# Optimization experiments

Measured on AMD Instinct MI355X. Metric: run time of the kernel, lower is better.

The kernel has to match this reference:

```python
import jax, jax.numpy as jnp
import numpy as np

B, M, K = 32, 64, 36
DS, DX, DQ, H = 512, 128, 512, 256


def setup_inputs() -> dict:
    key = jax.random.key(0)
    ks = jax.random.split(key, 11)
    sc = lambda fan_in: 1.0 / np.sqrt(fan_in)
    return {
        "s2": jax.random.normal(ks[0], (B, M, DS), jnp.float32),
        "x0": jax.random.normal(ks[1], (B, K, DX), jnp.float32),
        "q": jax.random.normal(ks[2], (B, DQ), jnp.float32),
        # score MLP: Linear(DS+DX+DQ -> H), ReLU, Linear(H -> 1)
        "score_w1": jax.random.normal(ks[3], (DS + DX + DQ, H), jnp.float32) * sc(DS + DX + DQ),
        "score_b1": jax.random.normal(ks[4], (H,), jnp.float32) * 0.01,
        "score_w2": jax.random.normal(ks[5], (H, 1), jnp.float32) * sc(H),
        "score_b2": jax.random.normal(ks[6], (1,), jnp.float32) * 0.01,
        # h MLP: Linear(DS -> H), ReLU, Linear(H -> DX)
        "h_w1": jax.random.normal(ks[7], (DS, H), jnp.float32) * sc(DS),
        "h_b1": jax.random.normal(ks[8], (H,), jnp.float32) * 0.01,
        "h_w2": jax.random.normal(ks[9], (H, DX), jnp.float32) * sc(H),
        "h_b2": jax.random.normal(ks[10], (DX,), jnp.float32) * 0.01,
    }


def reference(s2, x0, q, score_w1, score_b1, score_w2, score_b2, h_w1, h_b1, h_w2, h_b2):
    ds = s2.shape[-1]
    dx = x0.shape[-1]
    # First score Linear over concat [s_exp, x_exp, q_exp] decomposes into
    # block matmuls (same math as Linear on the concat, no 4D concat tensor).
    w_s = score_w1[:ds]            # (DS, H)
    w_x = score_w1[ds:ds + dx]     # (DX, H)
    w_q = score_w1[ds + dx:]       # (DQ, H)
    pre_s = jnp.einsum('bmd,dh->bmh', s2, w_s)   # (b, m, H)
    pre_x = jnp.einsum('bkd,dh->bkh', x0, w_x)   # (b, k, H)
    pre_q = q @ w_q                              # (b, H)
    hidden = jax.nn.relu(pre_s[:, :, None, :] + pre_x[:, None, :, :]
                         + pre_q[:, None, None, :] + score_b1)  # (b, m, k, H)
    logits = jnp.einsum('bmkh,h->bmk', hidden, score_w2[:, 0]) + score_b2[0]
    att = jax.nn.softmax(logits, axis=1)         # softmax over m
    h_s = jax.nn.relu(s2 @ h_w1 + h_b1) @ h_w2 + h_b2  # (b, m, DX)
    agg = jnp.einsum('bmk,bmf->bkf', att, h_s)   # (b, k, DX)
    return jnp.concatenate([x0, agg], axis=-1)   # (b, k, 2*DX)
```

## Files before the change

kernel.cpp:

```cpp
#include <hip/hip_runtime.h>

#define B_  32
#define M_  64
#define K_  36
#define DS_ 512
#define DX_ 128
#define DQ_ 512
#define H_  256

#define ROWS 8

__global__ __launch_bounds__(256) void kern1(
    const float* __restrict__ s2,
    const float* __restrict__ x0,
    const float* __restrict__ q,
    const float* __restrict__ score_w1,
    const float* __restrict__ score_b1,
    const float* __restrict__ h_w1,
    const float* __restrict__ h_b1,
    const float* __restrict__ h_w2,
    float* __restrict__ pre_s,
    float* __restrict__ px,
    float* __restrict__ qpre,
    float* __restrict__ hs)
{
    __shared__ float Ar[ROWS][H_];
    const int t   = threadIdx.x;
    const int bid = blockIdx.x;

    if (bid < 512) {
        const int tile = bid >> 1, mat = bid & 1;
        const float* W  = mat ? h_w1 : score_w1;
        const float* A  = s2 + (size_t)tile * ROWS * DS_;
        const float* Wp = W + t;

        float acc[ROWS];
        #pragma unroll
        for (int r = 0; r < ROWS; ++r) acc[r] = 0.f;

        #pragma unroll 2
        for (int k = 0; k < DS_; k += 4) {
            const float b0 = Wp[(size_t)(k + 0) * H_];
            const float b1 = Wp[(size_t)(k + 1) * H_];
            const float b2 = Wp[(size_t)(k + 2) * H_];
            const float b3 = Wp[(size_t)(k + 3) * H_];
            #pragma unroll
            for (int r = 0; r < ROWS; ++r) {
                const float4 a = *(const float4*)(A + (size_t)r * DS_ + k);
                acc[r] = fmaf(a.x, b0, acc[r]);
                acc[r] = fmaf(a.y, b1, acc[r]);
                acc[r] = fmaf(a.z, b2, acc[r]);
                acc[r] = fmaf(a.w, b3, acc[r]);
            }
        }

        if (!mat) {
            float* dst = pre_s + (size_t)tile * ROWS * H_ + t;
            #pragma unroll
            for (int r = 0; r < ROWS; ++r)
                dst[(size_t)r * H_] = acc[r];
        } else {
            const float b1v = h_b1[t];
            #pragma unroll
            for (int r = 0; r < ROWS; ++r)
                Ar[r][t] = fmaxf(acc[r] + b1v, 0.f);
            __syncthreads();

            const int f  = t & 127;
            const int rh = t >> 7;
            const float* w2p = h_w2 + f;
            float o0 = 0.f, o1 = 0.f, o2 = 0.f, o3 = 0.f;
            #pragma unroll 2
            for (int k = 0; k < H_; k += 4) {
                const float w0 = w2p[(size_t)(k + 0) * DX_];
                const float w1 = w2p[(size_t)(k + 1) * DX_];
                const float w2v = w2p[(size_t)(k + 2) * DX_];
                const float w3 = w2p[(size_t)(k + 3) * DX_];
                const float4 a0 = *(const float4*)&Ar[rh * 4 + 0][k];
                const float4 a1 = *(const float4*)&Ar[rh * 4 + 1][k];
                const float4 a2 = *(const float4*)&Ar[rh * 4 + 2][k];
                const float4 a3 = *(const float4*)&Ar[rh * 4 + 3][k];
                o0 = fmaf(a0.x, w0, o0); o0 = fmaf(a0.y, w1, o0);
                o0 = fmaf(a0.z, w2v, o0); o0 = fmaf(a0.w, w3, o0);
                o1 = fmaf(a1.x, w0, o1); o1 = fmaf(a1.y, w1, o1);
                o1 = fmaf(a1.z, w2v, o1); o1 = fmaf(a1.w, w3, o1);
                o2 = fmaf(a2.x, w0, o2); o2 = fmaf(a2.y, w1, o2);
                o2 = fmaf(a2.z, w2v, o2); o2 = fmaf(a2.w, w3, o2);
                o3 = fmaf(a3.x, w0, o3); o3 = fmaf(a3.y, w1, o3);
                o3 = fmaf(a3.z, w2v, o3); o3 = fmaf(a3.w, w3, o3);
            }
            float* dst = hs + ((size_t)tile * ROWS + rh * 4) * DX_ + f;
            dst[0 * DX_] = o0;
            dst[1 * DX_] = o1;
            dst[2 * DX_] = o2;
            dst[3 * DX_] = o3;
        }

    } else if (bid < 656) {
        const int tile = bid - 512;
        const float* A  = x0 + (size_t)tile * ROWS * DX_;
        const float* Wp = score_w1 + (size_t)DS_ * H_ + t;

        float acc[ROWS];
        #pragma unroll
        for (int r = 0; r < ROWS; ++r) acc[r] = 0.f;

        #pragma unroll 2
        for (int k = 0; k < DX_; k += 4) {
            const float b0 = Wp[(size_t)(k + 0) * H_];
            const float b1 = Wp[(size_t)(k + 1) * H_];
            const float b2 = Wp[(size_t)(k + 2) * H_];
            const float b3 = Wp[(size_t)(k + 3) * H_];
            #pragma unroll
            for (int r = 0; r < ROWS; ++r) {
                const float4 a = *(const float4*)(A + (size_t)r * DX_ + k);
                acc[r] = fmaf(a.x, b0, acc[r]);
                acc[r] = fmaf(a.y, b1, acc[r]);
                acc[r] = fmaf(a.z, b2, acc[r]);
                acc[r] = fmaf(a.w, b3, acc[r]);
            }
        }
        const float b1v = score_b1[t];
        float* dst = px + (size_t)tile * ROWS * H_ + t;
        #pragma unroll
        for (int r = 0; r < ROWS; ++r)
            dst[(size_t)r * H_] = acc[r] + b1v;

    } else {
        const int b = bid - 656;
        const float* qp = q + (size_t)b * DQ_;
        const float* wq = score_w1 + (size_t)(DS_ + DX_) * H_ + t;
        float a0 = 0.f, a1 = 0.f, a2 = 0.f, a3 = 0.f;
        #pragma unroll 2
        for (int d = 0; d < DQ_; d += 4) {
            const float4 q4 = *(const float4*)(qp + d);
            a0 = fmaf(q4.x, wq[(size_t)(d + 0) * H_], a0);
            a1 = fmaf(q4.y, wq[(size_t)(d + 1) * H_], a1);
            a2 = fmaf(q4.z, wq[(size_t)(d + 2) * H_], a2);
            a3 = fmaf(q4.w, wq[(size_t)(d + 3) * H_], a3);
        }
        qpre[(size_t)b * H_ + t] = (a0 + a1) + (a2 + a3);
    }
}

__global__ __launch_bounds__(256) void kern3(
    const float* __restrict__ pre_s,
    const float* __restrict__ px,
    const float* __restrict__ qpre,
    const float* __restrict__ score_w2,
    const float* __restrict__ hs,
    const float* __restrict__ h_b2,
    const float* __restrict__ x0,
    float* __restrict__ out)
{
    __shared__ float psf[M_ * H_];
    __shared__ float cw4[4][H_];
    __shared__ float att4[M_ * 4];
    __shared__ float pr[4][DX_];

    const int t   = threadIdx.x;
    const int b   = blockIdx.x / 9;
    const int k0  = (blockIdx.x % 9) * 4;
    const int bk0 = b * K_ + k0;

    const float* psrc = pre_s + (size_t)b * M_ * H_;
    #pragma unroll
    for (int i = 0; i < 16; ++i) {
        const int flat = t * 4 + i * 1024;
        const float4 v = *(const float4*)(psrc + flat);
        const int m = flat >> 8, hh = flat & 255;
        *(float4*)&psf[m * H_ + (hh ^ ((m & 7) << 2))] = v;
    }
    {
        const float qv = qpre[(size_t)b * H_ + t];
        #pragma unroll
        for (int kk = 0; kk < 4; ++kk)
            cw4[kk][t] = px[(size_t)(bk0 + kk) * H_ + t] + qv;
    }
    __syncthreads();

    {
        const int kk = t >> 6, m = t & 63;
        const int sw = (m & 7) << 2;
        const float* prow = &psf[m * H_];
        const float* crow = &cw4[kk][0];
        float lg = 0.f;
        for (int d = 0; d < 256; d += 4) {
            const float4 p = *(const float4*)&prow[d ^ sw];
            const float4 c = *(const float4*)&crow[d];
            const float4 v = *(const float4*)(score_w2 + d);
            lg += fmaxf(p.x + c.x, 0.f) * v.x + fmaxf(p.y + c.y, 0.f) * v.y
                + fmaxf(p.z + c.z, 0.f) * v.z + fmaxf(p.w + c.w, 0.f) * v.w;
        }
        float mx = lg;
        #pragma unroll
        for (int off = 32; off > 0; off >>= 1)
            mx = fmaxf(mx, __shfl_xor(mx, off, 64));
        const float e = expf(lg - mx);
        float sm = e;
        #pragma unroll
        for (int off = 32; off > 0; off >>= 1)
            sm += __shfl_xor(sm, off, 64);
        att4[m * 4 + kk] = e / sm;
    }
    __syncthreads();

    const int f = t & 127, half = t >> 7;
    {
        const float* hsp = hs + ((size_t)b * M_ + half * 32) * DX_ + f;
        float r0 = 0.f, r1 = 0.f, r2 = 0.f, r3 = 0.f;
        for (int m = 0; m < 32; ++m) {
            const float hv = hsp[(size_t)m * DX_];
            const float4 a = *(const float4*)&att4[(half * 32 + m) * 4];
            r0 = fmaf(a.x, hv, r0);
            r1 = fmaf(a.y, hv, r1);
            r2 = fmaf(a.z, hv, r2);
            r3 = fmaf(a.w, hv, r3);
        }
        if (half) {
            pr[0][f] = r0; pr[1][f] = r1; pr[2][f] = r2; pr[3][f] = r3;
        }
        __syncthreads();
        if (!half) {
            const float b2 = h_b2[f];
            out[(size_t)(bk0 + 0) * (2 * DX_) + DX_ + f] = r0 + pr[0][f] + b2;
            out[(size_t)(bk0 + 1) * (2 * DX_) + DX_ + f] = r1 + pr[1][f] + b2;
            out[(size_t)(bk0 + 2) * (2 * DX_) + DX_ + f] = r2 + pr[2][f] + b2;
            out[(size_t)(bk0 + 3) * (2 * DX_) + DX_ + f] = r3 + pr[3][f] + b2;
        }
    }
    #pragma unroll
    for (int j = 0; j < 2; ++j) {
        const int kk = half * 2 + j;
        out[(size_t)(bk0 + kk) * (2 * DX_) + f] = x0[(size_t)(bk0 + kk) * DX_ + f];
    }
}

extern "C" void kernel_launch(void* const* d_in, const int* in_sizes, int n_in,
                              void* d_out, int out_size, void* d_ws, size_t ws_size,
                              hipStream_t stream) {
    (void)in_sizes; (void)n_in; (void)out_size; (void)ws_size;
    const float* s2       = (const float*)d_in[0];
    const float* x0       = (const float*)d_in[1];
    const float* q        = (const float*)d_in[2];
    const float* score_w1 = (const float*)d_in[3];
    const float* score_b1 = (const float*)d_in[4];
    const float* score_w2 = (const float*)d_in[5];
    const float* h_w1     = (const float*)d_in[7];
    const float* h_b1     = (const float*)d_in[8];
    const float* h_w2     = (const float*)d_in[9];
    const float* h_b2     = (const float*)d_in[10];
    float* out = (float*)d_out;

    float* ws    = (float*)d_ws;
    float* pre_s = ws;
    float* px    = pre_s + (size_t)B_ * M_ * H_;
    float* qpre  = px    + (size_t)B_ * K_ * H_;
    float* hs    = qpre  + (size_t)B_ * H_;

    kern1<<<688, 256, 0, stream>>>(s2, x0, q, score_w1, score_b1, h_w1,
                                   h_b1, h_w2, pre_s, px, qpre, hs);
    kern3<<<288, 256, 0, stream>>>(pre_s, px, qpre, score_w2, hs, h_b2, x0, out);
}
```

Before: 133.3 us.

## Split-K projection blocks, separate h second layer, one block per (b,k) in attention

The projection kernel now uses 512-thread blocks that split the reduction dimension in half across two thread groups, handle 4 rows per block instead of 8, and combine the partial sums through shared memory. This gives many more blocks for better occupancy. The h-MLP second layer moves into its own kernel reading a ReLU'd intermediate from workspace. The attention kernel now runs one block per (b,k) with wave-parallel logit reductions instead of staging all of pre_s in shared memory. The cost is an extra launch, an extra intermediate buffer round-trip, and re-reading pre_s from global memory for each k.

```diff
diff --git a/kernel.cpp b/kernel.cpp
--- a/kernel.cpp
+++ b/kernel.cpp
@@ -8,9 +8,11 @@
 #define DQ_ 512
 #define H_  256
 
-#define ROWS 8
-
-__global__ __launch_bounds__(256) void kern1(
+#define S2B 1024
+#define PXB 288
+#define QPB 32
+
+__global__ __launch_bounds__(512, 6) void kern1(
     const float* __restrict__ s2,
     const float* __restrict__ x0,
     const float* __restrict__ q,
@@ -18,34 +20,35 @@
     const float* __restrict__ score_b1,
     const float* __restrict__ h_w1,
     const float* __restrict__ h_b1,
-    const float* __restrict__ h_w2,
     float* __restrict__ pre_s,
+    float* __restrict__ h1r,
     float* __restrict__ px,
-    float* __restrict__ qpre,
-    float* __restrict__ hs)
+    float* __restrict__ qpre)
 {
-    __shared__ float Ar[ROWS][H_];
+    __shared__ float comb[4 * H_];
     const int t   = threadIdx.x;
     const int bid = blockIdx.x;
-
-    if (bid < 512) {
+    const int h   = t & 255;
+    const int kh  = __builtin_amdgcn_readfirstlane(t >> 8);
+
+    if (bid < S2B) {
         const int tile = bid >> 1, mat = bid & 1;
         const float* W  = mat ? h_w1 : score_w1;
-        const float* A  = s2 + (size_t)tile * ROWS * DS_;
-        const float* Wp = W + t;
-
-        float acc[ROWS];
-        #pragma unroll
-        for (int r = 0; r < ROWS; ++r) acc[r] = 0.f;
+        const float* A  = s2 + (size_t)tile * 4 * DS_ + kh * 256;
+        const float* Wp = W + (size_t)(kh * 256) * H_ + h;
+
+        float acc[4];
+        #pragma unroll
+        for (int r = 0; r < 4; ++r) acc[r] = 0.f;
 
         #pragma unroll 2
-        for (int k = 0; k < DS_; k += 4) {
+        for (int k = 0; k < 256; k += 4) {
             const float b0 = Wp[(size_t)(k + 0) * H_];
             const float b1 = Wp[(size_t)(k + 1) * H_];
             const float b2 = Wp[(size_t)(k + 2) * H_];
             const float b3 = Wp[(size_t)(k + 3) * H_];
             #pragma unroll
-            for (int r = 0; r < ROWS; ++r) {
+            for (int r = 0; r < 4; ++r) {
                 const float4 a = *(const float4*)(A + (size_t)r * DS_ + k);
                 acc[r] = fmaf(a.x, b0, acc[r]);
                 acc[r] = fmaf(a.y, b1, acc[r]);
@@ -53,66 +56,44 @@
                 acc[r] = fmaf(a.w, b3, acc[r]);
             }
         }
-
-        if (!mat) {
-            float* dst = pre_s + (size_t)tile * ROWS * H_ + t;
-            #pragma unroll
-            for (int r = 0; r < ROWS; ++r)
-                dst[(size_t)r * H_] = acc[r];
-        } else {
-            const float b1v = h_b1[t];
-            #pragma unroll
-            for (int r = 0; r < ROWS; ++r)
-                Ar[r][t] = fmaxf(acc[r] + b1v, 0.f);
-            __syncthreads();
-
-            const int f  = t & 127;
-            const int rh = t >> 7;
-            const float* w2p = h_w2 + f;
-            float o0 = 0.f, o1 = 0.f, o2 = 0.f, o3 = 0.f;
-            #pragma unroll 2
-            for (int k = 0; k < H_; k += 4) {
-                const float w0 = w2p[(size_t)(k + 0) * DX_];
-                const float w1 = w2p[(size_t)(k + 1) * DX_];
-                const float w2v = w2p[(size_t)(k + 2) * DX_];
-                const float w3 = w2p[(size_t)(k + 3) * DX_];
-                const float4 a0 = *(const float4*)&Ar[rh * 4 + 0][k];
-                const float4 a1 = *(const float4*)&Ar[rh * 4 + 1][k];
-                const float4 a2 = *(const float4*)&Ar[rh * 4 + 2][k];
-                const float4 a3 = *(const float4*)&Ar[rh * 4 + 3][k];
-                o0 = fmaf(a0.x, w0, o0); o0 = fmaf(a0.y, w1, o0);
-                o0 = fmaf(a0.z, w2v, o0); o0 = fmaf(a0.w, w3, o0);
-                o1 = fmaf(a1.x, w0, o1); o1 = fmaf(a1.y, w1, o1);
-                o1 = fmaf(a1.z, w2v, o1); o1 = fmaf(a1.w, w3, o1);
-                o2 = fmaf(a2.x, w0, o2); o2 = fmaf(a2.y, w1, o2);
-                o2 = fmaf(a2.z, w2v, o2); o2 = fmaf(a2.w, w3, o2);
-                o3 = fmaf(a3.x, w0, o3); o3 = fmaf(a3.y, w1, o3);
-                o3 = fmaf(a3.z, w2v, o3); o3 = fmaf(a3.w, w3, o3);
+        if (kh) {
+            #pragma unroll
+            for (int r = 0; r < 4; ++r) comb[r * H_ + h] = acc[r];
+        }
+        __syncthreads();
+        if (!kh) {
+            if (!mat) {
+                float* dst = pre_s + (size_t)tile * 4 * H_ + h;
+                #pragma unroll
+                for (int r = 0; r < 4; ++r)
+                    dst[(size_t)r * H_] = acc[r] + comb[r * H_ + h];
+            } else {
+                const float b1v = h_b1[h];
+                float* dst = h1r + (size_t)tile * 4 * H_ + h;
+                #pragma unroll
+                for (int r = 0; r < 4; ++r)
+                    dst[(size_t)r * H_] =
+                        fmaxf(acc[r] + comb[r * H_ + h] + b1v, 0.f);
             }
-            float* dst = hs + ((size_t)tile * ROWS + rh * 4) * DX_ + f;
-            dst[0 * DX_] = o0;
-            dst[1 * DX_] = o1;
-            dst[2 * DX_] = o2;
-            dst[3 * DX_] = o3;
-        }
-
-    } else if (bid < 656) {
-        const int tile = bid - 512;
-        const float* A  = x0 + (size_t)tile * ROWS * DX_;
-        const float* Wp = score_w1 + (size_t)DS_ * H_ + t;
-
-        float acc[ROWS];
-        #pragma unroll
-        for (int r = 0; r < ROWS; ++r) acc[r] = 0.f;
+        }
+
+    } else if (bid < S2B + PXB) {
+        const int tile = bid - S2B;
+        const float* A  = x0 + (size_t)tile * 4 * DX_ + kh * 64;
+        const float* Wp = score_w1 + (size_t)(DS_ + kh * 64) * H_ + h;
+
+        float acc[4];
+        #pragma unroll
+        for (int r = 0; r < 4; ++r) acc[r] = 0.f;
 
         #pragma unroll 2
-        for (int k = 0; k < DX_; k += 4) {
+        for (int k = 0; k < 64; k += 4) {
             const float b0 = Wp[(size_t)(k + 0) * H_];
             const float b1 = Wp[(size_t)(k + 1) * H_];
             const float b2 = Wp[(size_t)(k + 2) * H_];
             const float b3 = Wp[(size_t)(k + 3) * H_];
             #pragma unroll
-            for (int r = 0; r < ROWS; ++r) {
+            for (int r = 0; r < 4; ++r) {
                 const float4 a = *(const float4*)(A + (size_t)r * DX_ + k);
                 acc[r] = fmaf(a.x, b0, acc[r]);
                 acc[r] = fmaf(a.y, b1, acc[r]);
@@ -120,27 +101,85 @@
                 acc[r] = fmaf(a.w, b3, acc[r]);
             }
         }
-        const float b1v = score_b1[t];
-        float* dst = px + (size_t)tile * ROWS * H_ + t;
-        #pragma unroll
-        for (int r = 0; r < ROWS; ++r)
-            dst[(size_t)r * H_] = acc[r] + b1v;
+        if (kh) {
+            #pragma unroll
+            for (int r = 0; r < 4; ++r) comb[r * H_ + h] = acc[r];
+        }
+        __syncthreads();
+        if (!kh) {
+            const float b1v = score_b1[h];
+            float* dst = px + (size_t)tile * 4 * H_ + h;
+            #pragma unroll
+            for (int r = 0; r < 4; ++r)
+                dst[(size_t)r * H_] = acc[r] + comb[r * H_ + h] + b1v;
+        }
 
     } else {
-        const int b = bid - 656;
-        const float* qp = q + (size_t)b * DQ_;
-        const float* wq = score_w1 + (size_t)(DS_ + DX_) * H_ + t;
+        const int b = bid - (S2B + PXB);
+        const float* qp = q + (size_t)b * DQ_ + kh * 256;
+        const float* wq = score_w1 + (size_t)(DS_ + DX_ + kh * 256) * H_ + h;
         float a0 = 0.f, a1 = 0.f, a2 = 0.f, a3 = 0.f;
         #pragma unroll 2
-        for (int d = 0; d < DQ_; d += 4) {
+        for (int d = 0; d < 256; d += 4) {
             const float4 q4 = *(const float4*)(qp + d);
             a0 = fmaf(q4.x, wq[(size_t)(d + 0) * H_], a0);
             a1 = fmaf(q4.y, wq[(size_t)(d + 1) * H_], a1);
             a2 = fmaf(q4.z, wq[(size_t)(d + 2) * H_], a2);
             a3 = fmaf(q4.w, wq[(size_t)(d + 3) * H_], a3);
         }
-        qpre[(size_t)b * H_ + t] = (a0 + a1) + (a2 + a3);
-    }
+        const float s = (a0 + a1) + (a2 + a3);
+        if (kh) comb[h] = s;
+        __syncthreads();
+        if (!kh) qpre[(size_t)b * H_ + h] = s + comb[h];
+    }
+}
+
+__global__ __launch_bounds__(256) void kern2(
+    const float* __restrict__ h1r,
+    const float* __restrict__ h_w2,
+    float* __restrict__ hs)
+{
+    __shared__ float A[8 * H_];
+    const int t  = threadIdx.x;
+    const int r0 = blockIdx.x * 8;
+
+    #pragma unroll
+    for (int i = 0; i < 2; ++i) {
+        const int flat = t * 4 + i * 1024;
+        *(float4*)&A[flat] = *(const float4*)(h1r + (size_t)r0 * H_ + flat);
+    }
+    __syncthreads();
+
+    const int f  = t & 127;
+    const int rg = t >> 7;
+    const float* Ar  = &A[rg * 4 * H_];
+    const float* w2p = h_w2 + f;
+
+    float o0 = 0.f, o1 = 0.f, o2 = 0.f, o3 = 0.f;
+    #pragma unroll 2
+    for (int k = 0; k < H_; k += 4) {
+        const float w0  = w2p[(size_t)(k + 0) * DX_];
+        const float w1  = w2p[(size_t)(k + 1) * DX_];
+        const float w2v = w2p[(size_t)(k + 2) * DX_];
+        const float w3  = w2p[(size_t)(k + 3) * DX_];
+        const float4 a0 = *(const float4*)&Ar[0 * H_ + k];
+        const float4 a1 = *(const float4*)&Ar[1 * H_ + k];
+        const float4 a2 = *(const float4*)&Ar[2 * H_ + k];
+        const float4 a3 = *(const float4*)&Ar[3 * H_ + k];
+        o0 = fmaf(a0.x, w0, o0); o0 = fmaf(a0.y, w1, o0);
+        o0 = fmaf(a0.z, w2v, o0); o0 = fmaf(a0.w, w3, o0);
+        o1 = fmaf(a1.x, w0, o1); o1 = fmaf(a1.y, w1, o1);
+        o1 = fmaf(a1.z, w2v, o1); o1 = fmaf(a1.w, w3, o1);
+        o2 = fmaf(a2.x, w0, o2); o2 = fmaf(a2.y, w1, o2);
+        o2 = fmaf(a2.z, w2v, o2); o2 = fmaf(a2.w, w3, o2);
+        o3 = fmaf(a3.x, w0, o3); o3 = fmaf(a3.y, w1, o3);
+        o3 = fmaf(a3.z, w2v, o3); o3 = fmaf(a3.w, w3, o3);
+    }
+    float* dst = hs + ((size_t)r0 + rg * 4) * DX_ + f;
+    dst[0 * DX_] = o0;
+    dst[1 * DX_] = o1;
+    dst[2 * DX_] = o2;
+    dst[3 * DX_] = o3;
 }
 
 __global__ __launch_bounds__(256) void kern3(
@@ -153,87 +192,70 @@
     const float* __restrict__ x0,
     float* __restrict__ out)
 {
-    __shared__ float psf[M_ * H_];
-    __shared__ float cw4[4][H_];
-    __shared__ float att4[M_ * 4];
-    __shared__ float pr[4][DX_];
-
-    const int t   = threadIdx.x;
-    const int b   = blockIdx.x / 9;
-    const int k0  = (blockIdx.x % 9) * 4;
-    const int bk0 = b * K_ + k0;
-
-    const float* psrc = pre_s + (size_t)b * M_ * H_;
-    #pragma unroll
-    for (int i = 0; i < 16; ++i) {
-        const int flat = t * 4 + i * 1024;
-        const float4 v = *(const float4*)(psrc + flat);
-        const int m = flat >> 8, hh = flat & 255;
-        *(float4*)&psf[m * H_ + (hh ^ ((m & 7) << 2))] = v;
-    }
+    __shared__ float logit[M_];
+    __shared__ float att[M_];
+    __shared__ float pr[DX_];
+
+    const int t    = threadIdx.x;
+    const int bk   = blockIdx.x;
+    const int b    = bk / K_;
+    const int lane = t & 63, wave = t >> 6;
+    const int hq   = lane << 2;
+
+    float4 c4, v4;
     {
-        const float qv = qpre[(size_t)b * H_ + t];
-        #pragma unroll
-        for (int kk = 0; kk < 4; ++kk)
-            cw4[kk][t] = px[(size_t)(bk0 + kk) * H_ + t] + qv;
+        const float4 qv = *(const float4*)(qpre + (size_t)b * H_ + hq);
+        const float4 pv = *(const float4*)(px + (size_t)bk * H_ + hq);
+        c4.x = qv.x + pv.x; c4.y = qv.y + pv.y;
+        c4.z = qv.z + pv.z; c4.w = qv.w + pv.w;
+        v4 = *(const float4*)(score_w2 + hq);
+    }
+
+    const float* ps = pre_s + (size_t)b * M_ * H_;
+    #pragma unroll 2
+    for (int mi = 0; mi < 16; ++mi) {
+        const int m = wave * 16 + mi;
+        const float4 p = *(const float4*)(ps + (size_t)m * H_ + hq);
+        float x = fmaxf(p.x + c4.x, 0.f) * v4.x
+                + fmaxf(p.y + c4.y, 0.f) * v4.y
+                + fmaxf(p.z + c4.z, 0.f) * v4.z
+                + fmaxf(p.w + c4.w, 0.f) * v4.w;
+        #pragma unroll
+        for (int off = 32; off > 0; off >>= 1)
+            x += __shfl_xor(x, off, 64);
+        if (lane == 0) logit[m] = x;
     }
     __syncthreads();
 
-    {
-        const int kk = t >> 6, m = t & 63;
-        const int sw = (m & 7) << 2;
-        const float* prow = &psf[m * H_];
-        const float* crow = &cw4[kk][0];
-        float lg = 0.f;
-        for (int d = 0; d < 256; d += 4) {
-            const float4 p = *(const float4*)&prow[d ^ sw];
-            const float4 c = *(const float4*)&crow[d];
-            const float4 v = *(const float4*)(score_w2 + d);
-            lg += fmaxf(p.x + c.x, 0.f) * v.x + fmaxf(p.y + c.y, 0.f) * v.y
-                + fmaxf(p.z + c.z, 0.f) * v.z + fmaxf(p.w + c.w, 0.f) * v.w;
-        }
-        float mx = lg;
+    if (wave == 0) {
+        const float L = logit[lane];
+        float mx = L;
         #pragma unroll
         for (int off = 32; off > 0; off >>= 1)
             mx = fmaxf(mx, __shfl_xor(mx, off, 64));
-        const float e = expf(lg - mx);
+        const float e = expf(L - mx);
         float sm = e;
         #pragma unroll
         for (int off = 32; off > 0; off >>= 1)
             sm += __shfl_xor(sm, off, 64);
-        att4[m * 4 + kk] = e / sm;
+        att[lane] = e / sm;
     }
     __syncthreads();
 
-    const int f = t & 127, half = t >> 7;
+    const int f = t & 127, mh = t >> 7;
     {
-        const float* hsp = hs + ((size_t)b * M_ + half * 32) * DX_ + f;
-        float r0 = 0.f, r1 = 0.f, r2 = 0.f, r3 = 0.f;
-        for (int m = 0; m < 32; ++m) {
-            const float hv = hsp[(size_t)m * DX_];
-            const float4 a = *(const float4*)&att4[(half * 32 + m) * 4];
-            r0 = fmaf(a.x, hv, r0);
-            r1 = fmaf(a.y, hv, r1);
-            r2 = fmaf(a.z, hv, r2);
-            r3 = fmaf(a.w, hv, r3);
-        }
-        if (half) {
-            pr[0][f] = r0; pr[1][f] = r1; pr[2][f] = r2; pr[3][f] = r3;
-        }
-        __syncthreads();
-        if (!half) {
-            const float b2 = h_b2[f];
-            out[(size_t)(bk0 + 0) * (2 * DX_) + DX_ + f] = r0 + pr[0][f] + b2;
-            out[(size_t)(bk0 + 1) * (2 * DX_) + DX_ + f] = r1 + pr[1][f] + b2;
-            out[(size_t)(bk0 + 2) * (2 * DX_) + DX_ + f] = r2 + pr[2][f] + b2;
-            out[(size_t)(bk0 + 3) * (2 * DX_) + DX_ + f] = r3 + pr[3][f] + b2;
-        }
-    }
-    #pragma unroll
-    for (int j = 0; j < 2; ++j) {
-        const int kk = half * 2 + j;
-        out[(size_t)(bk0 + kk) * (2 * DX_) + f] = x0[(size_t)(bk0 + kk) * DX_ + f];
-    }
+        const float* hsp = hs + ((size_t)b * M_ + mh * 32) * DX_ + f;
+        float r = 0.f;
+        #pragma unroll 4
+        for (int m2 = 0; m2 < 32; ++m2)
+            r = fmaf(att[mh * 32 + m2], hsp[(size_t)m2 * DX_], r);
+        if (mh) pr[f] = r;
+        __syncthreads();
+        if (!mh)
+            out[(size_t)bk * (2 * DX_) + DX_ + f] = r + pr[f] + h_b2[f];
+    }
+    if (t < DX_)
+        out[(size_t)bk * (2 * DX_) + t] = x0[(size_t)bk * DX_ + t];
 }
 
 extern "C" void kernel_launch(void* const* d_in, const int* in_sizes, int n_in,
@@ -254,11 +276,14 @@
 
     float* ws    = (float*)d_ws;
     float* pre_s = ws;
-    float* px    = pre_s + (size_t)B_ * M_ * H_;
+    float* h1r   = pre_s + (size_t)B_ * M_ * H_;
+    float* px    = h1r   + (size_t)B_ * M_ * H_;
     float* qpre  = px    + (size_t)B_ * K_ * H_;
     float* hs    = qpre  + (size_t)B_ * H_;
 
-    kern1<<<688, 256, 0, stream>>>(s2, x0, q, score_w1, score_b1, h_w1,
-                                   h_b1, h_w2, pre_s, px, qpre, hs);
-    kern3<<<288, 256, 0, stream>>>(pre_s, px, qpre, score_w2, hs, h_b2, x0, out);
-}
+    kern1<<<S2B + PXB + QPB, 512, 0, stream>>>(
+        s2, x0, q, score_w1, score_b1, h_w1, h_b1, pre_s, h1r, px, qpre);
+    kern2<<<256, 256, 0, stream>>>(h1r, h_w2, hs);
+    kern3<<<B_ * K_, 256, 0, stream>>>(pre_s, px, qpre, score_w2, hs, h_b2,
+                                       x0, out);
+}
```

Result: faster. 128.5 us (-3.6%).
